# Kernel optimization log

Measured on AMD Instinct MI355X. Metric: run time of the kernel, lower is better.

Reference implementation:

```python
import jax, jax.numpy as jnp
import numpy as np

# EctConfig constants
RESOLUTION = 64   # number of threshold steps
RADIUS = 1.1      # thresholds span [-RADIUS, RADIUS]
NUM_BATCHES = 64  # number of point clouds


def setup_inputs() -> dict:
    key = jax.random.key(0)
    k1, k2, k3 = jax.random.split(key, 3)
    N, D, T = 1048576, 3, 64
    x = jax.random.normal(k1, (N, D), dtype=jnp.float32) * 0.5  # points roughly inside radius
    v = jax.random.normal(k2, (D, T), dtype=jnp.float32)
    v = v / jnp.linalg.norm(v, axis=0, keepdims=True)  # unit directions [D, T]
    batch = jnp.sort(jax.random.randint(k3, (N,), 0, NUM_BATCHES)).astype(jnp.int64)
    return {"x": x, "v": v, "batch": batch, "num_batches": NUM_BATCHES}


def reference(x, v, batch, num_batches):
    # Projection of every point onto every direction: [N, T]
    nh = x @ v
    R = RESOLUTION
    T = v.shape[1]
    # Map each projected height to a threshold bin in [0, R-1]
    bins = jnp.clip(
        jnp.floor((nh + RADIUS) / (2.0 * RADIUS) * R), 0, R - 1
    ).astype(jnp.int32)  # [N, T]
    # Fused (batch, bin) index so a single scatter-add builds all histograms
    flat = batch[:, None].astype(jnp.int32) * R + bins  # [N, T]
    counts = jnp.zeros((num_batches * R, T), dtype=jnp.float32)
    counts = counts.at[flat, jnp.arange(T)[None, :]].add(1.0)
    # Cumulative count over thresholds = Euler characteristic curve per direction
    ect = jnp.cumsum(counts.reshape(num_batches, R, T), axis=1)  # [B, R, T]
    return ect
```

## Files before the change

kernel.cpp:

```cpp
#include <hip/hip_runtime.h>

#define RES 64
#define TD 64
#define NB 64
#define BLK 1024
#define WAVES 16
#define CHUNK 2048

__global__ __launch_bounds__(256) void ect_init_kernel(
    const int* __restrict__ batch, int N,
    unsigned* __restrict__ counts, int* __restrict__ offs)
{
    int gid = blockIdx.x * 256 + threadIdx.x;
    counts[gid] = 0u;
    if (blockIdx.x == 0 && threadIdx.x <= NB) {
        int val = (int)threadIdx.x;
        int lo = 0, hi = N;
        while (lo < hi) {
            int mid = (lo + hi) >> 1;
            if (batch[mid] < val) lo = mid + 1; else hi = mid;
        }
        offs[threadIdx.x] = lo;
    }
}

__global__ __launch_bounds__(BLK) void ect_hist_kernel(
    const float* __restrict__ x, const float* __restrict__ v,
    const int* __restrict__ offs, unsigned* __restrict__ counts, int N)
{
    const int start = blockIdx.x * CHUNK;
    const int stop  = min(start + CHUNK, N);
    if (start >= N) return;

    __shared__ unsigned hist[2][RES * TD];

    const int t = threadIdx.x & 63;
    const int w = threadIdx.x >> 6;
    unsigned* __restrict__ hw = hist[w >> 3];
    const float S = 64.0f / 2.2f;
    const float v0S = v[t] * S;
    const float v1S = v[TD + t] * S;
    const float v2S = v[2 * TD + t] * S;

    int lo = 0, hi = NB;
    while (lo < hi) {
        int mid = (lo + hi + 1) >> 1;
        if (offs[mid] <= start) lo = mid; else hi = mid - 1;
    }
    int b = lo;

#define SELREG(q, r0, r1, r2) ((q) < 64 ? (r0) : ((q) < 128 ? (r1) : (r2)))
#define RD(q, r0, r1, r2) __uint_as_float(__builtin_amdgcn_readlane(           \
        __float_as_uint(SELREG(q, r0, r1, r2)), (q) & 63))
#define PROC1(j, r0, r1, r2) {                                                 \
        float x0 = RD(3*(j), r0,r1,r2), x1 = RD(3*(j)+1, r0,r1,r2),            \
              x2 = RD(3*(j)+2, r0,r1,r2);                                      \
        float f = fmaf(x0, v0S, fmaf(x1, v1S, fmaf(x2, v2S, 32.0f)));          \
        f = __builtin_amdgcn_fmed3f(f, 0.0f, 63.0f);                           \
        int bin = (int)f;                                                      \
        atomicAdd(&hw[(bin << 6) + t], 1u); }

    int seg = start;
    while (seg < stop) {
        while (offs[b + 1] <= seg) ++b;
        const int segend = min(stop, offs[b + 1]);

        for (int i = threadIdx.x; i < 2 * RES * TD; i += BLK) hist[0][i] = 0u;
        __syncthreads();

        const int npts = segend - seg;
        const int nf = npts >> 6;

        float c0, c1, c2, n0, n1, n2;
        int tl = w;
        if (tl < nf) {
            const int fb = 3 * (seg + (tl << 6)) + t;
            c0 = x[fb]; c1 = x[fb + 64]; c2 = x[fb + 128];
        }
        for (; tl < nf; tl += WAVES) {
            const int tn = tl + WAVES;
            if (tn < nf) {
                const int fb = 3 * (seg + (tn << 6)) + t;
                n0 = x[fb]; n1 = x[fb + 64]; n2 = x[fb + 128];
            }
            #pragma unroll
            for (int j = 0; j < 64; ++j) PROC1(j, c0, c1, c2);
            if (tn < nf) { c0 = n0; c1 = n1; c2 = n2; }
        }

        const int rem = npts & 63;
        if (rem && w == (nf & (WAVES - 1))) {
            const int fb = 3 * (seg + (nf << 6)) + t;
            const int lim = 3 * segend;
            float l0 = (fb       < lim) ? x[fb]       : 0.0f;
            float l1 = (fb +  64 < lim) ? x[fb +  64] : 0.0f;
            float l2 = (fb + 128 < lim) ? x[fb + 128] : 0.0f;
            #pragma unroll
            for (int j = 0; j < 64; ++j) {
                if (j < rem) PROC1(j, l0, l1, l2);
            }
        }
        __syncthreads();

        unsigned* __restrict__ gb = counts + b * (RES * TD);
        for (int i = threadIdx.x; i < RES * TD; i += BLK) {
            unsigned h = hist[0][i] + hist[1][i];
            if (h) atomicAdd(&gb[i], h);
        }
        if (segend < stop) __syncthreads();
        seg = segend;
    }
#undef PROC1
#undef RD
#undef SELREG
}

__global__ __launch_bounds__(64) void ect_cumsum_kernel(unsigned* __restrict__ u)
{
    int b = blockIdx.x, t = threadIdx.x;
    int base = b * (RES * TD) + t;

    unsigned vals[RES];
    #pragma unroll
    for (int r = 0; r < RES; ++r) vals[r] = u[base + (r << 6)];

    unsigned acc = 0u;
    #pragma unroll
    for (int r = 0; r < RES; ++r) {
        acc += vals[r];
        u[base + (r << 6)] = __float_as_uint((float)acc);
    }
}

extern "C" void kernel_launch(void* const* d_in, const int* in_sizes, int n_in,
                              void* d_out, int out_size, void* d_ws, size_t ws_size,
                              hipStream_t stream) {
    const float* x = (const float*)d_in[0];
    const float* v = (const float*)d_in[1];
    const int* batch = (const int*)d_in[2];
    const int N = in_sizes[2];
    int* offs = (int*)d_ws;

    ect_init_kernel<<<(NB * RES * TD) / 256, 256, 0, stream>>>(
        batch, N, (unsigned*)d_out, offs);

    const int nblocks = (N + CHUNK - 1) / CHUNK;
    ect_hist_kernel<<<nblocks, BLK, 0, stream>>>(x, v, offs, (unsigned*)d_out, N);

    ect_cumsum_kernel<<<NB, 64, 0, stream>>>((unsigned*)d_out);
}
```

Measured before the change: 33.89 us.

## Fuse cumulative sum into histogram kernel via per-block prefix and float atomics

Removes the separate cumsum kernel. Each block computes a prefix sum over bins of its local histogram, using per-wave partial sums in shared memory, then atomically adds the float cumulative counts straight into the output. The init kernel is vectorized to clear the output with float4 stores. In exchange, every block now issues a float atomic for all bins, since zero bins are no longer skipped once cumulative. It also adds an extra barrier, and float atomics are exact only while counts stay below 2^24.

New measurement: 32.74 us. -3.4%, faster.

```diff
diff --git a/kernel.cpp b/kernel.cpp
--- a/kernel.cpp
+++ b/kernel.cpp
@@ -9,10 +9,10 @@
 
 __global__ __launch_bounds__(256) void ect_init_kernel(
     const int* __restrict__ batch, int N,
-    unsigned* __restrict__ counts, int* __restrict__ offs)
+    float4* __restrict__ out4, int* __restrict__ offs)
 {
     int gid = blockIdx.x * 256 + threadIdx.x;
-    counts[gid] = 0u;
+    out4[gid] = float4{0.f, 0.f, 0.f, 0.f};
     if (blockIdx.x == 0 && threadIdx.x <= NB) {
         int val = (int)threadIdx.x;
         int lo = 0, hi = N;
@@ -26,17 +26,18 @@
 
 __global__ __launch_bounds__(BLK) void ect_hist_kernel(
     const float* __restrict__ x, const float* __restrict__ v,
-    const int* __restrict__ offs, unsigned* __restrict__ counts, int N)
+    const int* __restrict__ offs, float* __restrict__ out, int N)
 {
     const int start = blockIdx.x * CHUNK;
     const int stop  = min(start + CHUNK, N);
     if (start >= N) return;
 
     __shared__ unsigned hist[2][RES * TD];
+    __shared__ unsigned col_part[TD][17];
 
     const int t = threadIdx.x & 63;
     const int w = threadIdx.x >> 6;
-    unsigned* __restrict__ hw = hist[w >> 3];
+    unsigned* __restrict__ hwt = &hist[w >> 3][t];
     const float S = 64.0f / 2.2f;
     const float v0S = v[t] * S;
     const float v1S = v[TD + t] * S;
@@ -58,7 +59,7 @@
         float f = fmaf(x0, v0S, fmaf(x1, v1S, fmaf(x2, v2S, 32.0f)));          \
         f = __builtin_amdgcn_fmed3f(f, 0.0f, 63.0f);                           \
         int bin = (int)f;                                                      \
-        atomicAdd(&hw[(bin << 6) + t], 1u); }
+        atomicAdd(hwt + (bin << 6), 1u); }
 
     int seg = start;
     while (seg < stop) {
@@ -102,10 +103,27 @@
         }
         __syncthreads();
 
-        unsigned* __restrict__ gb = counts + b * (RES * TD);
-        for (int i = threadIdx.x; i < RES * TD; i += BLK) {
-            unsigned h = hist[0][i] + hist[1][i];
-            if (h) atomicAdd(&gb[i], h);
+        unsigned vals[4];
+        {
+            unsigned s = 0;
+            #pragma unroll
+            for (int i = 0; i < 4; ++i) {
+                int r = (w << 2) + i;
+                s += hist[0][(r << 6) + t] + hist[1][(r << 6) + t];
+                vals[i] = s;
+            }
+            col_part[t][w] = s;
+        }
+        __syncthreads();
+        {
+            unsigned off = 0;
+            for (int j = 0; j < w; ++j) off += col_part[t][j];
+            float* __restrict__ gb = out + b * (RES * TD) + t;
+            #pragma unroll
+            for (int i = 0; i < 4; ++i) {
+                int r = (w << 2) + i;
+                atomicAdd(gb + (r << 6), (float)(vals[i] + off));
+            }
         }
         if (segend < stop) __syncthreads();
         seg = segend;
@@ -113,23 +131,6 @@
 #undef PROC1
 #undef RD
 #undef SELREG
-}
-
-__global__ __launch_bounds__(64) void ect_cumsum_kernel(unsigned* __restrict__ u)
-{
-    int b = blockIdx.x, t = threadIdx.x;
-    int base = b * (RES * TD) + t;
-
-    unsigned vals[RES];
-    #pragma unroll
-    for (int r = 0; r < RES; ++r) vals[r] = u[base + (r << 6)];
-
-    unsigned acc = 0u;
-    #pragma unroll
-    for (int r = 0; r < RES; ++r) {
-        acc += vals[r];
-        u[base + (r << 6)] = __float_as_uint((float)acc);
-    }
 }
 
 extern "C" void kernel_launch(void* const* d_in, const int* in_sizes, int n_in,
@@ -141,11 +142,9 @@
     const int N = in_sizes[2];
     int* offs = (int*)d_ws;
 
-    ect_init_kernel<<<(NB * RES * TD) / 256, 256, 0, stream>>>(
-        batch, N, (unsigned*)d_out, offs);
+    ect_init_kernel<<<(NB * RES * TD) / (256 * 4), 256, 0, stream>>>(
+        batch, N, (float4*)d_out, offs);
 
     const int nblocks = (N + CHUNK - 1) / CHUNK;
-    ect_hist_kernel<<<nblocks, BLK, 0, stream>>>(x, v, offs, (unsigned*)d_out, N);
-
-    ect_cumsum_kernel<<<NB, 64, 0, stream>>>((unsigned*)d_out);
+    ect_hist_kernel<<<nblocks, BLK, 0, stream>>>(x, v, offs, (float*)d_out, N);
 }
```
